# Performance work log

Measured on AMD Instinct MI355X. Metric: run time of the kernel, lower is better.

The kernel has to match this reference:

```python
import jax, jax.numpy as jnp
import numpy as np

N_NODES = 100000
N_EDGES = 1600000
DIM = 64          # dim_in = dim_out
DIM3 = 3 * DIM    # concat(X_src, X_dst, E)


def _linear_params(key, fan_in, fan_out):
    kw, kb = jax.random.split(key)
    s = 1.0 / np.sqrt(fan_in)
    W = jax.random.uniform(kw, (fan_in, fan_out), jnp.float32, -s, s)
    b = jax.random.uniform(kb, (fan_out,), jnp.float32, -s, s)
    return W, b


def setup_inputs() -> dict:
    key = jax.random.key(0)
    ks = jax.random.split(key, 8)
    X = jax.random.normal(ks[0], (N_NODES, DIM), jnp.float32)
    E = jax.random.normal(ks[1], (N_EDGES, DIM), jnp.float32)
    emb_nodes = jnp.zeros((N_NODES, DIM), jnp.float32)
    emb_edges = jnp.zeros((N_EDGES, DIM), jnp.float32)
    edge_index = jax.random.randint(ks[2], (2, N_EDGES), 0, N_NODES, jnp.int64)
    # mlp_att: [192, 48, 24, 1]  (dims: dim_in3, max(dim_in3//4,16), max(dim_in3//8,4), 1)
    aw1, ab1 = _linear_params(ks[3], DIM3, max(DIM3 // 4, 16))
    aw2, ab2 = _linear_params(ks[4], max(DIM3 // 4, 16), max(DIM3 // 8, 4))
    aw3, ab3 = _linear_params(ks[5], max(DIM3 // 8, 4), 1)
    # mlp_msg: [192, 128, 64]  (dims: dim_in3, (dim_in3+dim_out)//2, dim_out)
    mw1, mb1 = _linear_params(ks[6], DIM3, (DIM3 + DIM) // 2)
    mw2, mb2 = _linear_params(ks[7], (DIM3 + DIM) // 2, DIM)
    return {"X": X, "E": E, "emb_nodes": emb_nodes, "emb_edges": emb_edges,
            "edge_index": edge_index,
            "aw1": aw1, "ab1": ab1, "aw2": aw2, "ab2": ab2, "aw3": aw3, "ab3": ab3,
            "mw1": mw1, "mb1": mb1, "mw2": mw2, "mb2": mb2}


def reference(X, E, emb_nodes, emb_edges, edge_index,
              aw1, ab1, aw2, ab2, aw3, ab3, mw1, mb1, mw2, mb2):
    src, dst = edge_index[0], edge_index[1]
    # H: [n_edges, 3*dim]
    H = jnp.concatenate([X[src], X[dst], E], axis=-1)
    # attention gate MLP -> [n_edges, 1]
    a = jax.nn.relu(H @ aw1 + ab1)
    a = jax.nn.relu(a @ aw2 + ab2)
    a = a @ aw3 + ab3
    # message MLP -> [n_edges, dim_out]
    m = jax.nn.relu(H @ mw1 + mb1)
    m = m @ mw2 + mb2
    M = jax.nn.sigmoid(a) * m
    X_out = X + jax.ops.segment_sum(M, dst, num_segments=X.shape[0])
    return X_out
```

## Files before the change

### kernel.cpp

```cpp
#include <hip/hip_runtime.h>
#include <math.h>


typedef __attribute__((ext_vector_type(4))) short short4v;
typedef __attribute__((ext_vector_type(8))) short short8v;
typedef __attribute__((ext_vector_type(4))) float float4v;

#define RS 400
#define RA 80

#define OFF_W1T 0
#define OFF_W2T 73728
#define OFF_W3T 90112
#define OFF_B1  94208
#define OFF_AB2 95040
#define OFF_AW3 95168

static __device__ __forceinline__ short f2bf(float f) {
    union { float f; unsigned u; } v; v.f = f;
    unsigned r = (v.u + 0x7fffu + ((v.u >> 16) & 1u)) >> 16;
    return (short)r;
}
static __device__ __forceinline__ float bf2f(short s) {
    union { unsigned u; float f; } v; v.u = ((unsigned)(unsigned short)s) << 16;
    return v.f;
}

__global__ __launch_bounds__(256) void copy_kernel(const float4* __restrict__ src,
                                                   float4* __restrict__ dst, int n4) {
    int i = blockIdx.x * 256 + threadIdx.x;
    if (i < n4) dst[i] = src[i];
}

__global__ __launch_bounds__(256) void prep_kernel(
    const float* __restrict__ mw1, const float* __restrict__ aw1,
    const float* __restrict__ mw2, const float* __restrict__ aw2,
    const float* __restrict__ mb1, const float* __restrict__ ab1,
    const float* __restrict__ ab2, const float* __restrict__ aw3,
    char* __restrict__ ws)
{
    unsigned short* W1T = (unsigned short*)(ws + OFF_W1T);
    unsigned short* W2T = (unsigned short*)(ws + OFF_W2T);
    unsigned short* W3T = (unsigned short*)(ws + OFF_W3T);
    float* B1  = (float*)(ws + OFF_B1);
    float* AB2 = (float*)(ws + OFF_AB2);
    float* AW3 = (float*)(ws + OFF_AW3);

    int i = blockIdx.x * 256 + threadIdx.x;
    const int n1 = 192 * 192;
    const int n2 = 64 * 128;
    const int n3 = 32 * 64;
    if (i < n1) {
        int j = i / 192, k = i % 192;
        float v = 0.f;
        if (j < 128)      v = mw1[(size_t)k * 128 + j];
        else if (j < 176) v = aw1[(size_t)k * 48 + (j - 128)];
        W1T[i] = (unsigned short)f2bf(v);
    } else if (i < n1 + n2) {
        int r = i - n1; int j = r >> 7, k = r & 127;
        W2T[r] = (unsigned short)f2bf(mw2[(size_t)k * 64 + j]);
    } else if (i < n1 + n2 + n3) {
        int r = i - n1 - n2; int j = r >> 6, k = r & 63;
        float v = (j < 24 && k < 48) ? aw2[(size_t)k * 24 + j] : 0.f;
        W3T[r] = (unsigned short)f2bf(v);
    } else if (i < n1 + n2 + n3 + 208) {
        int j = i - n1 - n2 - n3;
        float v = 0.f;
        if (j < 128)      v = mb1[j];
        else if (j < 176) v = ab1[j - 128];
        B1[j] = v;
    } else if (i < n1 + n2 + n3 + 208 + 32) {
        int j = i - n1 - n2 - n3 - 208;
        AB2[j] = (j < 24) ? ab2[j] : 0.f;
    } else if (i < n1 + n2 + n3 + 208 + 64) {
        int k = i - n1 - n2 - n3 - 208 - 32;
        AW3[k] = (k < 24) ? aw3[k] : 0.f;
    }
}

__global__ __launch_bounds__(256) void edge_kernel(
    const float* __restrict__ X, const float* __restrict__ E,
    const int* __restrict__ eidx, const char* __restrict__ ws,
    const float* __restrict__ ab3, const float* __restrict__ mb2,
    float* __restrict__ Xout, int n_edges)
{
    const unsigned short* W1T = (const unsigned short*)(ws + OFF_W1T);
    const unsigned short* W2T = (const unsigned short*)(ws + OFF_W2T);
    const unsigned short* W3T = (const unsigned short*)(ws + OFF_W3T);
    const float* B1  = (const float*)(ws + OFF_B1);
    const float* AB2 = (const float*)(ws + OFF_AB2);
    const float* AW3 = (const float*)(ws + OFF_AW3);

    extern __shared__ char smem[];
    int*   si   = (int*)smem;
    int*   di   = (int*)(smem + 256);
    float* gate = (float*)(smem + 512);
    char*  a2s  = smem + 768;
    char*  Hs   = smem + 768 + 5120;

    const int t    = threadIdx.x;
    const int w    = t >> 6;
    const int lane = t & 63;
    const int n16  = lane & 15;
    const int q    = lane >> 4;
    const int e0   = blockIdx.x * 64;

    if (t < 64) {
        int eg = e0 + t; if (eg >= n_edges) eg = n_edges - 1;
        si[t] = eidx[eg];
        di[t] = eidx[n_edges + eg];
    }
    __syncthreads();

    #pragma unroll
    for (int s = 0; s < 3; s++) {
        #pragma unroll
        for (int i = 0; i < 4; i++) {
            int idx = i * 256 + t;
            int e = idx >> 4, k = (idx & 15) * 4;
            const float* p;
            if (s == 0)      p = X + (size_t)si[e] * 64 + k;
            else if (s == 1) p = X + (size_t)di[e] * 64 + k;
            else { int ee = e0 + e; if (ee >= n_edges) ee = n_edges - 1;
                   p = E + (size_t)ee * 64 + k; }
            float4 v = *(const float4*)p;
            short4v b; b[0] = f2bf(v.x); b[1] = f2bf(v.y); b[2] = f2bf(v.z); b[3] = f2bf(v.w);
            *(short4v*)(Hs + e * RS + (s * 64 + k) * 2) = b;
        }
    }
    __syncthreads();

    float4v acc1[3][4];
    #pragma unroll
    for (int a = 0; a < 3; a++)
        #pragma unroll
        for (int b = 0; b < 4; b++)
            acc1[a][b] = (float4v){0.f, 0.f, 0.f, 0.f};

    #pragma unroll
    for (int ks = 0; ks < 6; ks++) {
        short8v af[4];
        #pragma unroll
        for (int et = 0; et < 4; et++)
            af[et] = *(const short8v*)(Hs + (et * 16 + n16) * RS + (ks * 32 + q * 8) * 2);
        #pragma unroll
        for (int ji = 0; ji < 3; ji++) {
            int jt = w + ji * 4;
            short8v bf = *(const short8v*)(W1T + (size_t)(jt * 16 + n16) * 192 + ks * 32 + q * 8);
            #pragma unroll
            for (int et = 0; et < 4; et++)
                acc1[ji][et] = __builtin_amdgcn_mfma_f32_16x16x32_bf16(af[et], bf, acc1[ji][et], 0, 0, 0);
        }
    }
    __syncthreads();

    #pragma unroll
    for (int ji = 0; ji < 3; ji++) {
        int jt = w + ji * 4;
        int j  = jt * 16 + n16;
        float bias = B1[j];
        #pragma unroll
        for (int et = 0; et < 4; et++) {
            #pragma unroll
            for (int r = 0; r < 4; r++) {
                int e = et * 16 + q * 4 + r;
                float v = fmaxf(acc1[ji][et][r] + bias, 0.f);
                *(short*)(Hs + e * RS + j * 2) = f2bf(v);
            }
        }
    }
    __syncthreads();

    float4v acc2[4];
    float4v acc3[2];
    #pragma unroll
    for (int a = 0; a < 4; a++) acc2[a] = (float4v){0.f, 0.f, 0.f, 0.f};
    #pragma unroll
    for (int a = 0; a < 2; a++) acc3[a] = (float4v){0.f, 0.f, 0.f, 0.f};

    #pragma unroll
    for (int ks = 0; ks < 4; ks++) {
        short8v bf = *(const short8v*)(W2T + (size_t)(w * 16 + n16) * 128 + ks * 32 + q * 8);
        #pragma unroll
        for (int et = 0; et < 4; et++) {
            short8v af = *(const short8v*)(Hs + (et * 16 + n16) * RS + (ks * 32 + q * 8) * 2);
            acc2[et] = __builtin_amdgcn_mfma_f32_16x16x32_bf16(af, bf, acc2[et], 0, 0, 0);
        }
    }
    #pragma unroll
    for (int ks = 0; ks < 2; ks++) {
        short8v af = *(const short8v*)(Hs + (w * 16 + n16) * RS + 256 + ks * 64 + q * 16);
        #pragma unroll
        for (int jt2 = 0; jt2 < 2; jt2++) {
            short8v bf = *(const short8v*)(W3T + (size_t)(jt2 * 16 + n16) * 64 + ks * 32 + q * 8);
            acc3[jt2] = __builtin_amdgcn_mfma_f32_16x16x32_bf16(af, bf, acc3[jt2], 0, 0, 0);
        }
    }

    #pragma unroll
    for (int jt2 = 0; jt2 < 2; jt2++) {
        int j = jt2 * 16 + n16;
        float bias = AB2[j];
        #pragma unroll
        for (int r = 0; r < 4; r++) {
            int e = w * 16 + q * 4 + r;
            float v = fmaxf(acc3[jt2][r] + bias, 0.f);
            *(short*)(a2s + e * RA + j * 2) = f2bf(v);
        }
    }
    __syncthreads();

    if (t < 64) {
        short8v r0 = *(const short8v*)(a2s + t * RA);
        short8v r1 = *(const short8v*)(a2s + t * RA + 16);
        short8v r2 = *(const short8v*)(a2s + t * RA + 32);
        float s = ab3[0];
        #pragma unroll
        for (int k = 0; k < 8; k++) s = fmaf(bf2f(r0[k]), AW3[k], s);
        #pragma unroll
        for (int k = 0; k < 8; k++) s = fmaf(bf2f(r1[k]), AW3[8 + k], s);
        #pragma unroll
        for (int k = 0; k < 8; k++) s = fmaf(bf2f(r2[k]), AW3[16 + k], s);
        gate[t] = 1.f / (1.f + expf(-s));
    }
    __syncthreads();

    {
        int j = w * 16 + n16;
        float bias = mb2[j];
        #pragma unroll
        for (int et = 0; et < 4; et++) {
            #pragma unroll
            for (int r = 0; r < 4; r++) {
                int e = et * 16 + q * 4 + r;
                if (e0 + e < n_edges) {
                    float g = gate[e];
                    atomicAdd(Xout + (size_t)di[e] * 64 + j, (acc2[et][r] + bias) * g);
                }
            }
        }
    }
}

extern "C" void kernel_launch(void* const* d_in, const int* in_sizes, int n_in,
                              void* d_out, int out_size, void* d_ws, size_t ws_size,
                              hipStream_t stream) {
    const float* X   = (const float*)d_in[0];
    const float* E   = (const float*)d_in[1];
    const int*   eidx= (const int*)d_in[4];
    const float* aw1 = (const float*)d_in[5];
    const float* ab1 = (const float*)d_in[6];
    const float* aw2 = (const float*)d_in[7];
    const float* ab2 = (const float*)d_in[8];
    const float* aw3 = (const float*)d_in[9];
    const float* ab3 = (const float*)d_in[10];
    const float* mw1 = (const float*)d_in[11];
    const float* mb1 = (const float*)d_in[12];
    const float* mw2 = (const float*)d_in[13];
    const float* mb2 = (const float*)d_in[14];
    float* Xout = (float*)d_out;

    int n_node_elems = in_sizes[0];
    int n_edges      = in_sizes[1] / 64;

    int n4 = n_node_elems / 4;
    copy_kernel<<<(n4 + 255) / 256, 256, 0, stream>>>((const float4*)X, (float4*)Xout, n4);

    prep_kernel<<<(192 * 192 + 64 * 128 + 32 * 64 + 208 + 64 + 255) / 256, 256, 0, stream>>>(
        mw1, aw1, mw2, aw2, mb1, ab1, ab2, aw3, (char*)d_ws);

    int ntiles = (n_edges + 63) / 64;
    size_t shmem = 768 + 5120 + 64 * RS;
    edge_kernel<<<ntiles, 256, shmem, stream>>>(X, E, eidx, (const char*)d_ws,
                                                ab3, mb2, Xout, n_edges);
}
```

Measured before the change: 1.271 ms.

## Make edge kernel persistent with register-resident weights and double-buffered gather prefetch

The edge kernel now runs as a persistent grid of 512 blocks that loop over edge tiles. Each block loads the W1/W2/W3 bf16 fragments and biases into registers once instead of once per tile. It double-buffers the H tile in shared memory and keeps a triple-buffered ring of edge indices, so the gather for the next tile is issued before the current tile's MFMA work starts, hiding gather latency. The costs are much higher register pressure from the resident weight fragments, larger shared memory per block (about 58 KB), and a fixed grid size that may underfill or unbalance the GPU.

```diff
diff --git a/kernel.cpp b/kernel.cpp
--- a/kernel.cpp
+++ b/kernel.cpp
@@ -8,6 +8,7 @@
 
 #define RS 400
 #define RA 80
+#define NBLK 512
 
 #define OFF_W1T 0
 #define OFF_W2T 73728
@@ -25,6 +26,7 @@
     union { unsigned u; float f; } v; v.u = ((unsigned)(unsigned short)s) << 16;
     return v.f;
 }
+static __device__ __forceinline__ int imin(int a, int b) { return a < b ? a : b; }
 
 __global__ __launch_bounds__(256) void copy_kernel(const float4* __restrict__ src,
                                                    float4* __restrict__ dst, int n4) {
@@ -47,9 +49,7 @@
     float* AW3 = (float*)(ws + OFF_AW3);
 
     int i = blockIdx.x * 256 + threadIdx.x;
-    const int n1 = 192 * 192;
-    const int n2 = 64 * 128;
-    const int n3 = 32 * 64;
+    const int n1 = 192 * 192, n2 = 64 * 128, n3 = 32 * 64;
     if (i < n1) {
         int j = i / 192, k = i % 192;
         float v = 0.f;
@@ -78,7 +78,7 @@
     }
 }
 
-__global__ __launch_bounds__(256) void edge_kernel(
+__global__ __launch_bounds__(256, 2) void edge_kernel(
     const float* __restrict__ X, const float* __restrict__ E,
     const int* __restrict__ eidx, const char* __restrict__ ws,
     const float* __restrict__ ab3, const float* __restrict__ mb2,
@@ -93,152 +93,221 @@
 
     extern __shared__ char smem[];
     int*   si   = (int*)smem;
-    int*   di   = (int*)(smem + 256);
-    float* gate = (float*)(smem + 512);
-    char*  a2s  = smem + 768;
-    char*  Hs   = smem + 768 + 5120;
+    int*   di   = (int*)(smem + 768);
+    float* gate = (float*)(smem + 1536);
+    char*  a2s  = smem + 1792;
+    char*  Hs0  = smem + 6912;
+    char*  Hs1  = smem + 32512;
 
     const int t    = threadIdx.x;
     const int w    = t >> 6;
     const int lane = t & 63;
     const int n16  = lane & 15;
     const int q    = lane >> 4;
-    const int e0   = blockIdx.x * 64;
-
-    if (t < 64) {
-        int eg = e0 + t; if (eg >= n_edges) eg = n_edges - 1;
-        si[t] = eidx[eg];
-        di[t] = eidx[n_edges + eg];
-    }
-    __syncthreads();
-
-    #pragma unroll
-    for (int s = 0; s < 3; s++) {
-        #pragma unroll
-        for (int i = 0; i < 4; i++) {
-            int idx = i * 256 + t;
-            int e = idx >> 4, k = (idx & 15) * 4;
-            const float* p;
-            if (s == 0)      p = X + (size_t)si[e] * 64 + k;
-            else if (s == 1) p = X + (size_t)di[e] * 64 + k;
-            else { int ee = e0 + e; if (ee >= n_edges) ee = n_edges - 1;
-                   p = E + (size_t)ee * 64 + k; }
-            float4 v = *(const float4*)p;
-            short4v b; b[0] = f2bf(v.x); b[1] = f2bf(v.y); b[2] = f2bf(v.z); b[3] = f2bf(v.w);
-            *(short4v*)(Hs + e * RS + (s * 64 + k) * 2) = b;
-        }
-    }
-    __syncthreads();
-
-    float4v acc1[3][4];
-    #pragma unroll
-    for (int a = 0; a < 3; a++)
-        #pragma unroll
-        for (int b = 0; b < 4; b++)
-            acc1[a][b] = (float4v){0.f, 0.f, 0.f, 0.f};
-
-    #pragma unroll
-    for (int ks = 0; ks < 6; ks++) {
-        short8v af[4];
-        #pragma unroll
-        for (int et = 0; et < 4; et++)
-            af[et] = *(const short8v*)(Hs + (et * 16 + n16) * RS + (ks * 32 + q * 8) * 2);
-        #pragma unroll
-        for (int ji = 0; ji < 3; ji++) {
-            int jt = w + ji * 4;
-            short8v bf = *(const short8v*)(W1T + (size_t)(jt * 16 + n16) * 192 + ks * 32 + q * 8);
-            #pragma unroll
-            for (int et = 0; et < 4; et++)
-                acc1[ji][et] = __builtin_amdgcn_mfma_f32_16x16x32_bf16(af[et], bf, acc1[ji][et], 0, 0, 0);
-        }
-    }
-    __syncthreads();
-
+    const int ntiles = (n_edges + 63) >> 6;
+    const int nb = gridDim.x;
+
+    int tile = blockIdx.x;
+    if (tile >= ntiles) return;
+
+    short8v w1f[3][6];
+    float   b1m[3];
     #pragma unroll
     for (int ji = 0; ji < 3; ji++) {
         int jt = w + ji * 4;
-        int j  = jt * 16 + n16;
-        float bias = B1[j];
-        #pragma unroll
-        for (int et = 0; et < 4; et++) {
-            #pragma unroll
-            for (int r = 0; r < 4; r++) {
-                int e = et * 16 + q * 4 + r;
-                float v = fmaxf(acc1[ji][et][r] + bias, 0.f);
-                *(short*)(Hs + e * RS + j * 2) = f2bf(v);
-            }
-        }
-    }
-    __syncthreads();
-
-    float4v acc2[4];
-    float4v acc3[2];
+        #pragma unroll
+        for (int ks = 0; ks < 6; ks++)
+            w1f[ji][ks] = *(const short8v*)(W1T + (size_t)(jt * 16 + n16) * 192 + ks * 32 + q * 8);
+        b1m[ji] = B1[jt * 16 + n16];
+    }
+    short8v w2f[4];
     #pragma unroll
-    for (int a = 0; a < 4; a++) acc2[a] = (float4v){0.f, 0.f, 0.f, 0.f};
-    #pragma unroll
-    for (int a = 0; a < 2; a++) acc3[a] = (float4v){0.f, 0.f, 0.f, 0.f};
-
-    #pragma unroll
-    for (int ks = 0; ks < 4; ks++) {
-        short8v bf = *(const short8v*)(W2T + (size_t)(w * 16 + n16) * 128 + ks * 32 + q * 8);
-        #pragma unroll
-        for (int et = 0; et < 4; et++) {
-            short8v af = *(const short8v*)(Hs + (et * 16 + n16) * RS + (ks * 32 + q * 8) * 2);
-            acc2[et] = __builtin_amdgcn_mfma_f32_16x16x32_bf16(af, bf, acc2[et], 0, 0, 0);
-        }
-    }
-    #pragma unroll
-    for (int ks = 0; ks < 2; ks++) {
-        short8v af = *(const short8v*)(Hs + (w * 16 + n16) * RS + 256 + ks * 64 + q * 16);
-        #pragma unroll
-        for (int jt2 = 0; jt2 < 2; jt2++) {
-            short8v bf = *(const short8v*)(W3T + (size_t)(jt2 * 16 + n16) * 64 + ks * 32 + q * 8);
-            acc3[jt2] = __builtin_amdgcn_mfma_f32_16x16x32_bf16(af, bf, acc3[jt2], 0, 0, 0);
-        }
-    }
-
+    for (int ks = 0; ks < 4; ks++)
+        w2f[ks] = *(const short8v*)(W2T + (size_t)(w * 16 + n16) * 128 + ks * 32 + q * 8);
+    short8v w3f[2][2];
+    float   ab2v[2];
     #pragma unroll
     for (int jt2 = 0; jt2 < 2; jt2++) {
-        int j = jt2 * 16 + n16;
-        float bias = AB2[j];
-        #pragma unroll
-        for (int r = 0; r < 4; r++) {
-            int e = w * 16 + q * 4 + r;
-            float v = fmaxf(acc3[jt2][r] + bias, 0.f);
-            *(short*)(a2s + e * RA + j * 2) = f2bf(v);
-        }
+        #pragma unroll
+        for (int ks = 0; ks < 2; ks++)
+            w3f[jt2][ks] = *(const short8v*)(W3T + (size_t)(jt2 * 16 + n16) * 64 + ks * 32 + q * 8);
+        ab2v[jt2] = AB2[jt2 * 16 + n16];
+    }
+    const float mb2v = mb2[w * 16 + n16];
+    const float ab3v = ab3[0];
+
+    const int eb = t >> 4;
+    const int k4 = (t & 15) * 4;
+
+    if (t < 64) {
+        int a0 = imin(tile * 64 + t, n_edges - 1);
+        int t1 = imin(tile + nb, ntiles - 1);
+        int a1 = imin(t1 * 64 + t, n_edges - 1);
+        si[t]      = eidx[a0];  di[t]      = eidx[n_edges + a0];
+        si[64 + t] = eidx[a1];  di[64 + t] = eidx[n_edges + a1];
     }
     __syncthreads();
-
-    if (t < 64) {
-        short8v r0 = *(const short8v*)(a2s + t * RA);
-        short8v r1 = *(const short8v*)(a2s + t * RA + 16);
-        short8v r2 = *(const short8v*)(a2s + t * RA + 32);
-        float s = ab3[0];
-        #pragma unroll
-        for (int k = 0; k < 8; k++) s = fmaf(bf2f(r0[k]), AW3[k], s);
-        #pragma unroll
-        for (int k = 0; k < 8; k++) s = fmaf(bf2f(r1[k]), AW3[8 + k], s);
-        #pragma unroll
-        for (int k = 0; k < 8; k++) s = fmaf(bf2f(r2[k]), AW3[16 + k], s);
-        gate[t] = 1.f / (1.f + expf(-s));
+    {
+        int e0 = tile * 64;
+        #pragma unroll
+        for (int i = 0; i < 4; i++) {
+            int e = i * 16 + eb;
+            float4 vx = *(const float4*)(X + (size_t)si[e] * 64 + k4);
+            float4 vy = *(const float4*)(X + (size_t)di[e] * 64 + k4);
+            float4 vz = *(const float4*)(E + (size_t)imin(e0 + e, n_edges - 1) * 64 + k4);
+            short4v b;
+            b[0]=f2bf(vx.x); b[1]=f2bf(vx.y); b[2]=f2bf(vx.z); b[3]=f2bf(vx.w);
+            *(short4v*)(Hs0 + e * RS + k4 * 2) = b;
+            b[0]=f2bf(vy.x); b[1]=f2bf(vy.y); b[2]=f2bf(vy.z); b[3]=f2bf(vy.w);
+            *(short4v*)(Hs0 + e * RS + 128 + k4 * 2) = b;
+            b[0]=f2bf(vz.x); b[1]=f2bf(vz.y); b[2]=f2bf(vz.z); b[3]=f2bf(vz.w);
+            *(short4v*)(Hs0 + e * RS + 256 + k4 * 2) = b;
+        }
     }
     __syncthreads();
 
-    {
-        int j = w * 16 + n16;
-        float bias = mb2[j];
-        #pragma unroll
-        for (int et = 0; et < 4; et++) {
+    char* cur = Hs0;
+    char* nxt = Hs1;
+    int scur = 0;
+
+    for (; tile < ntiles; tile += nb) {
+        int snxt = scur + 1; if (snxt == 3) snxt = 0;
+        int spf  = snxt + 1; if (spf  == 3) spf  = 0;
+        int tnext = imin(tile + nb, ntiles - 1);
+        int tpf   = imin(tile + 2 * nb, ntiles - 1);
+
+        int pfs = 0, pfd = 0;
+        if (t < 64) {
+            int a = imin(tpf * 64 + t, n_edges - 1);
+            pfs = eidx[a];
+            pfd = eidx[n_edges + a];
+        }
+
+        float4 vx[4], vy[4], vz[4];
+        {
+            int e0n = tnext * 64;
+            #pragma unroll
+            for (int i = 0; i < 4; i++) {
+                int e = i * 16 + eb;
+                int es = si[snxt * 64 + e];
+                int ed = di[snxt * 64 + e];
+                vz[i] = *(const float4*)(E + (size_t)imin(e0n + e, n_edges - 1) * 64 + k4);
+                vx[i] = *(const float4*)(X + (size_t)es * 64 + k4);
+                vy[i] = *(const float4*)(X + (size_t)ed * 64 + k4);
+            }
+        }
+
+        float4v acc1[3][4];
+        #pragma unroll
+        for (int a = 0; a < 3; a++)
+            #pragma unroll
+            for (int b = 0; b < 4; b++)
+                acc1[a][b] = (float4v){0.f, 0.f, 0.f, 0.f};
+        #pragma unroll
+        for (int ks = 0; ks < 6; ks++) {
+            short8v af[4];
+            #pragma unroll
+            for (int et = 0; et < 4; et++)
+                af[et] = *(const short8v*)(cur + (et * 16 + n16) * RS + (ks * 32 + q * 8) * 2);
+            #pragma unroll
+            for (int ji = 0; ji < 3; ji++)
+                #pragma unroll
+                for (int et = 0; et < 4; et++)
+                    acc1[ji][et] = __builtin_amdgcn_mfma_f32_16x16x32_bf16(af[et], w1f[ji][ks], acc1[ji][et], 0, 0, 0);
+        }
+        __syncthreads();
+
+        #pragma unroll
+        for (int ji = 0; ji < 3; ji++) {
+            int j = (w + ji * 4) * 16 + n16;
+            float bias = b1m[ji];
+            #pragma unroll
+            for (int et = 0; et < 4; et++)
+                #pragma unroll
+                for (int r = 0; r < 4; r++) {
+                    int e = et * 16 + q * 4 + r;
+                    *(short*)(cur + e * RS + j * 2) = f2bf(fmaxf(acc1[ji][et][r] + bias, 0.f));
+                }
+        }
+        #pragma unroll
+        for (int i = 0; i < 4; i++) {
+            int e = i * 16 + eb;
+            short4v b;
+            b[0]=f2bf(vx[i].x); b[1]=f2bf(vx[i].y); b[2]=f2bf(vx[i].z); b[3]=f2bf(vx[i].w);
+            *(short4v*)(nxt + e * RS + k4 * 2) = b;
+            b[0]=f2bf(vy[i].x); b[1]=f2bf(vy[i].y); b[2]=f2bf(vy[i].z); b[3]=f2bf(vy[i].w);
+            *(short4v*)(nxt + e * RS + 128 + k4 * 2) = b;
+            b[0]=f2bf(vz[i].x); b[1]=f2bf(vz[i].y); b[2]=f2bf(vz[i].z); b[3]=f2bf(vz[i].w);
+            *(short4v*)(nxt + e * RS + 256 + k4 * 2) = b;
+        }
+        if (t < 64) { si[spf * 64 + t] = pfs; di[spf * 64 + t] = pfd; }
+        __syncthreads();
+
+        float4v acc2[4], acc3[2];
+        #pragma unroll
+        for (int a = 0; a < 4; a++) acc2[a] = (float4v){0.f, 0.f, 0.f, 0.f};
+        #pragma unroll
+        for (int a = 0; a < 2; a++) acc3[a] = (float4v){0.f, 0.f, 0.f, 0.f};
+        #pragma unroll
+        for (int ks = 0; ks < 4; ks++) {
+            #pragma unroll
+            for (int et = 0; et < 4; et++) {
+                short8v af = *(const short8v*)(cur + (et * 16 + n16) * RS + (ks * 32 + q * 8) * 2);
+                acc2[et] = __builtin_amdgcn_mfma_f32_16x16x32_bf16(af, w2f[ks], acc2[et], 0, 0, 0);
+            }
+        }
+        #pragma unroll
+        for (int ks = 0; ks < 2; ks++) {
+            short8v af = *(const short8v*)(cur + (w * 16 + n16) * RS + 256 + ks * 64 + q * 16);
+            #pragma unroll
+            for (int jt2 = 0; jt2 < 2; jt2++)
+                acc3[jt2] = __builtin_amdgcn_mfma_f32_16x16x32_bf16(af, w3f[jt2][ks], acc3[jt2], 0, 0, 0);
+        }
+        #pragma unroll
+        for (int jt2 = 0; jt2 < 2; jt2++) {
+            int j = jt2 * 16 + n16;
+            float bias = ab2v[jt2];
             #pragma unroll
             for (int r = 0; r < 4; r++) {
-                int e = et * 16 + q * 4 + r;
-                if (e0 + e < n_edges) {
-                    float g = gate[e];
-                    atomicAdd(Xout + (size_t)di[e] * 64 + j, (acc2[et][r] + bias) * g);
+                int e = w * 16 + q * 4 + r;
+                *(short*)(a2s + e * RA + j * 2) = f2bf(fmaxf(acc3[jt2][r] + bias, 0.f));
+            }
+        }
+        __syncthreads();
+
+        if (t < 64) {
+            short8v r0 = *(const short8v*)(a2s + t * RA);
+            short8v r1 = *(const short8v*)(a2s + t * RA + 16);
+            short8v r2 = *(const short8v*)(a2s + t * RA + 32);
+            float s = ab3v;
+            #pragma unroll
+            for (int k = 0; k < 8; k++) s = fmaf(bf2f(r0[k]), AW3[k], s);
+            #pragma unroll
+            for (int k = 0; k < 8; k++) s = fmaf(bf2f(r1[k]), AW3[8 + k], s);
+            #pragma unroll
+            for (int k = 0; k < 8; k++) s = fmaf(bf2f(r2[k]), AW3[16 + k], s);
+            gate[t] = 1.f / (1.f + expf(-s));
+        }
+        __syncthreads();
+
+        {
+            int j = w * 16 + n16;
+            int e0 = tile * 64;
+            #pragma unroll
+            for (int et = 0; et < 4; et++)
+                #pragma unroll
+                for (int r = 0; r < 4; r++) {
+                    int e = et * 16 + q * 4 + r;
+                    if (e0 + e < n_edges) {
+                        float g = gate[e];
+                        atomicAdd(Xout + (size_t)di[scur * 64 + e] * 64 + j,
+                                  (acc2[et][r] + mb2v) * g);
+                    }
                 }
-            }
-        }
+        }
+
+        char* tmp = cur; cur = nxt; nxt = tmp;
+        scur = snxt;
     }
 }
 
@@ -270,7 +339,8 @@
         mw1, aw1, mw2, aw2, mb1, ab1, ab2, aw3, (char*)d_ws);
 
     int ntiles = (n_edges + 63) / 64;
-    size_t shmem = 768 + 5120 + 64 * RS;
-    edge_kernel<<<ntiles, 256, shmem, stream>>>(X, E, eidx, (const char*)d_ws,
-                                                ab3, mb2, Xout, n_edges);
-}
+    int grid = NBLK < ntiles ? NBLK : ntiles;
+    size_t shmem = 58112;
+    edge_kernel<<<grid, 256, shmem, stream>>>(X, E, eidx, (const char*)d_ws,
+                                              ab3, mb2, Xout, n_edges);
+}
```

After: 1.074 ms. -15.5%, faster.
